# Kernel tuning notes

Hardware: AMD Instinct MI355X
Metric: run time of the kernel (lower is better)

## Reference

```python
import jax, jax.numpy as jnp
import numpy as np

B, S, H = 8, 2048, 768      # batch, seq_len, hidden_size
N = 512                     # spans per example
MAXW = 30                   # max span width (length in [0, MAXW-1] -> width <= MAXW)


def setup_inputs() -> dict:
    key = jax.random.key(0)
    k1, k2, k3, k4 = jax.random.split(key, 4)
    embeddings = jax.random.normal(k1, (B, S, H), dtype=jnp.float32)
    starts = jax.random.randint(k2, (B, N), 0, S - MAXW)          # span starts
    lengths = jax.random.randint(k3, (B, N), 0, MAXW)             # end = start + length
    w = jax.random.normal(k4, (H, 1), dtype=jnp.float32) * 0.02   # nn.Linear(hidden, 1) weight (transposed)
    b = jnp.zeros((1,), dtype=jnp.float32)                        # linear bias
    return {"embeddings": embeddings, "w": w, "b": b, "starts": starts, "lengths": lengths}


def reference(embeddings, w, b, starts, lengths):
    # Vectorized ragged span pooling: gather up to MAXW tokens per span,
    # masked softmax over attention scores, then concat [start, end, attn].
    ends = starts + lengths                                  # inclusive end index
    offs = jnp.arange(MAXW)                                  # (W,)
    positions = starts[..., None] + offs                     # (B, N, W)
    mask = offs[None, None, :] <= lengths[..., None]         # (B, N, W) valid-token mask

    gather = jax.vmap(lambda e, p: e[p])                     # per-example gather
    span_emb = gather(embeddings, positions)                 # (B, N, W, H)

    scores = span_emb @ w + b                                # (B, N, W, 1)
    scores = jnp.where(mask[..., None], scores, -jnp.inf)
    attn_w = jax.nn.softmax(scores, axis=2)                  # masked softmax over span width
    attn_out = jnp.sum(attn_w * span_emb, axis=2)            # (B, N, H)

    start_emb = gather(embeddings, starts)                   # (B, N, H)
    end_emb = gather(embeddings, ends)                       # (B, N, H)
    return jnp.concatenate([start_emb, end_emb, attn_out], axis=-1)  # (B, N, 3H)
```

## Files before the change

### kernel.cpp

```cpp
#include <hip/hip_runtime.h>
#include <hip/hip_bf16.h>
#include <math.h>

#define BB 8
#define SS 2048
#define HH 768
#define NN 512
#define MAXW 30
#define CK 6

__global__ __launch_bounds__(256) void sort_spans_kernel(
    const int* __restrict__ starts,
    int*       __restrict__ order)
{
    const int b   = blockIdx.x;
    const int tid = threadIdx.x;
    __shared__ int hist[SS];
    __shared__ int wsum[4];

    for (int i = tid; i < SS; i += 256) hist[i] = 0;
    __syncthreads();

    const int* st = starts + b * NN;
    for (int n = tid; n < NN; n += 256) atomicAdd(&hist[st[n]], 1);
    __syncthreads();

    const int base = tid * 8;
    int cnt[8]; int s = 0;
    #pragma unroll
    for (int k = 0; k < 8; ++k) { cnt[k] = hist[base + k]; s += cnt[k]; }

    const int lane = tid & 63, wv = tid >> 6;
    int v = s;
    #pragma unroll
    for (int off = 1; off < 64; off <<= 1) {
        int u = __shfl_up(v, off);
        if (lane >= off) v += u;
    }
    if (lane == 63) wsum[wv] = v;
    __syncthreads();
    int wbase = 0;
    #pragma unroll
    for (int k = 0; k < 4; ++k) wbase += (k < wv) ? wsum[k] : 0;

    int excl = wbase + v - s;
    #pragma unroll
    for (int k = 0; k < 8; ++k) { int c = cnt[k]; hist[base + k] = excl; excl += c; }
    __syncthreads();

    for (int n = tid; n < NN; n += 256) {
        int pos = atomicAdd(&hist[st[n]], 1);
        order[b * NN + pos] = n;
    }
}

__global__ __launch_bounds__(256) void span_fused_kernel(
    const float* __restrict__ emb,
    const float* __restrict__ w,
    const float* __restrict__ bias,
    const int*   __restrict__ starts,
    const int*   __restrict__ lengths,
    const int*   __restrict__ order,
    float*       __restrict__ out)
{
    const int tid  = threadIdx.x;
    const int wv   = tid >> 6;
    const int lane = tid & 63;
    const int bi   = blockIdx.x & 7;
    const int rank = ((int)blockIdx.x >> 3) * 4 + wv;
    const int n    = order ? order[bi * NN + rank] : rank;
    const int span = bi * NN + n;

    const int start = starts[span];
    const int len   = lengths[span];

    const float* ebase = emb + (size_t)bi * SS * HH + (size_t)start * HH;
    const int h0 = lane * 4;
    float* orow = out + (size_t)span * (3 * HH);

    const float4 w0 = *reinterpret_cast<const float4*>(w + h0);
    const float4 w1 = *reinterpret_cast<const float4*>(w + h0 + 256);
    const float4 w2 = *reinterpret_cast<const float4*>(w + h0 + 512);
    const float bb = bias[0];

    float m = -INFINITY, ssum = 0.f;
    float4 a0 = make_float4(0.f, 0.f, 0.f, 0.f), a1 = a0, a2 = a0;

    const int nchunks = (len + CK) / CK;

    for (int c = 0; c < nchunks; ++c) {
        const int tbase = c * CK;

        float4 r0[CK], r1[CK], r2[CK];
        #pragma unroll
        for (int k = 0; k < CK; ++k) {
            const float* rp = ebase + (size_t)(tbase + k) * HH;
            r0[k] = *reinterpret_cast<const float4*>(rp + h0);
            r1[k] = *reinterpret_cast<const float4*>(rp + h0 + 256);
            r2[k] = *reinterpret_cast<const float4*>(rp + h0 + 512);
        }

        float d[CK];
        #pragma unroll
        for (int k = 0; k < CK; ++k) {
            d[k] = r0[k].x * w0.x + r0[k].y * w0.y + r0[k].z * w0.z + r0[k].w * w0.w
                 + r1[k].x * w1.x + r1[k].y * w1.y + r1[k].z * w1.z + r1[k].w * w1.w
                 + r2[k].x * w2.x + r2[k].y * w2.y + r2[k].z * w2.z + r2[k].w * w2.w;
        }

        #pragma unroll
        for (int off = 32; off; off >>= 1) {
            #pragma unroll
            for (int k = 0; k < CK; ++k) d[k] += __shfl_xor(d[k], off);
        }

        #pragma unroll
        for (int k = 0; k < CK; ++k)
            d[k] = (tbase + k <= len) ? (d[k] + bb) : -INFINITY;

        float cmax = d[0];
        #pragma unroll
        for (int k = 1; k < CK; ++k) cmax = fmaxf(cmax, d[k]);
        if (cmax > m) {
            const float cc = __expf(m - cmax);
            ssum *= cc;
            a0.x *= cc; a0.y *= cc; a0.z *= cc; a0.w *= cc;
            a1.x *= cc; a1.y *= cc; a1.z *= cc; a1.w *= cc;
            a2.x *= cc; a2.y *= cc; a2.z *= cc; a2.w *= cc;
            m = cmax;
        }

        #pragma unroll
        for (int k = 0; k < CK; ++k) {
            const float pt = __expf(d[k] - m);
            ssum += pt;
            a0.x += pt * r0[k].x; a0.y += pt * r0[k].y; a0.z += pt * r0[k].z; a0.w += pt * r0[k].w;
            a1.x += pt * r1[k].x; a1.y += pt * r1[k].y; a1.z += pt * r1[k].z; a1.w += pt * r1[k].w;
            a2.x += pt * r2[k].x; a2.y += pt * r2[k].y; a2.z += pt * r2[k].z; a2.w += pt * r2[k].w;

            if (tbase + k == 0) {
                *reinterpret_cast<float4*>(orow + h0)       = r0[k];
                *reinterpret_cast<float4*>(orow + h0 + 256) = r1[k];
                *reinterpret_cast<float4*>(orow + h0 + 512) = r2[k];
            }
            if (tbase + k == len) {
                *reinterpret_cast<float4*>(orow + HH + h0)       = r0[k];
                *reinterpret_cast<float4*>(orow + HH + h0 + 256) = r1[k];
                *reinterpret_cast<float4*>(orow + HH + h0 + 512) = r2[k];
            }
        }
    }

    const float inv = 1.f / ssum;
    a0.x *= inv; a0.y *= inv; a0.z *= inv; a0.w *= inv;
    a1.x *= inv; a1.y *= inv; a1.z *= inv; a1.w *= inv;
    a2.x *= inv; a2.y *= inv; a2.z *= inv; a2.w *= inv;
    *reinterpret_cast<float4*>(orow + 2 * HH + h0)       = a0;
    *reinterpret_cast<float4*>(orow + 2 * HH + h0 + 256) = a1;
    *reinterpret_cast<float4*>(orow + 2 * HH + h0 + 512) = a2;
}

extern "C" void kernel_launch(void* const* d_in, const int* in_sizes, int n_in,
                              void* d_out, int out_size, void* d_ws, size_t ws_size,
                              hipStream_t stream) {
    const float* emb     = (const float*)d_in[0];
    const float* w       = (const float*)d_in[1];
    const float* bias    = (const float*)d_in[2];
    const int*   starts  = (const int*)d_in[3];
    const int*   lengths = (const int*)d_in[4];
    float*       out     = (float*)d_out;

    int* order = nullptr;
    if (ws_size >= (size_t)(BB * NN * sizeof(int))) {
        order = (int*)d_ws;
        sort_spans_kernel<<<dim3(BB), dim3(256), 0, stream>>>(starts, order);
    }

    span_fused_kernel<<<dim3(BB * NN / 4), dim3(256), 0, stream>>>(
        emb, w, bias, starts, lengths, order, out);
}
```

Measured before the change: 34.87 us.

## Group 8 sorted spans per block and sweep their shared token union in lockstep

Each block now handles 8 start-sorted spans (one per wave, 512 threads) instead of 4. The block computes the min start and max end over its spans, and all waves step over that token range together in chunks of 4, with a block barrier after each chunk. Each wave loads only tokens inside its own span, so overlapping spans hit the same rows close together in time, which should raise cache reuse. In exchange, waves whose spans are short or far apart run many empty iterations and wait at every barrier. The chunk shrinks from 6 to 4 tokens, which reduces memory-level parallelism per wave.

```diff
diff --git a/kernel.cpp b/kernel.cpp
--- a/kernel.cpp
+++ b/kernel.cpp
@@ -7,7 +7,8 @@
 #define HH 768
 #define NN 512
 #define MAXW 30
-#define CK 6
+#define SPW 8
+#define CH  4
 
 __global__ __launch_bounds__(256) void sort_spans_kernel(
     const int* __restrict__ starts,
@@ -54,7 +55,7 @@
     }
 }
 
-__global__ __launch_bounds__(256) void span_fused_kernel(
+__global__ __launch_bounds__(512, 4) void span_union_kernel(
     const float* __restrict__ emb,
     const float* __restrict__ w,
     const float* __restrict__ bias,
@@ -67,14 +68,23 @@
     const int wv   = tid >> 6;
     const int lane = tid & 63;
     const int bi   = blockIdx.x & 7;
-    const int rank = ((int)blockIdx.x >> 3) * 4 + wv;
+    const int g    = (int)blockIdx.x >> 3;
+    const int rank = g * SPW + wv;
     const int n    = order ? order[bi * NN + rank] : rank;
     const int span = bi * NN + n;
 
     const int start = starts[span];
     const int len   = lengths[span];
-
-    const float* ebase = emb + (size_t)bi * SS * HH + (size_t)start * HH;
+    const int end   = start + len;
+
+    __shared__ int s_lo[SPW], s_hi[SPW];
+    if (lane == 0) { s_lo[wv] = start; s_hi[wv] = end; }
+    __syncthreads();
+    int wlo = s_lo[0], whi = s_hi[0];
+    #pragma unroll
+    for (int k = 1; k < SPW; ++k) { wlo = min(wlo, s_lo[k]); whi = max(whi, s_hi[k]); }
+
+    const float* ebase = emb + (size_t)bi * SS * HH;
     const int h0 = lane * 4;
     float* orow = out + (size_t)span * (3 * HH);
 
@@ -86,41 +96,47 @@
     float m = -INFINITY, ssum = 0.f;
     float4 a0 = make_float4(0.f, 0.f, 0.f, 0.f), a1 = a0, a2 = a0;
 
-    const int nchunks = (len + CK) / CK;
-
-    for (int c = 0; c < nchunks; ++c) {
-        const int tbase = c * CK;
-
-        float4 r0[CK], r1[CK], r2[CK];
-        #pragma unroll
-        for (int k = 0; k < CK; ++k) {
-            const float* rp = ebase + (size_t)(tbase + k) * HH;
-            r0[k] = *reinterpret_cast<const float4*>(rp + h0);
-            r1[k] = *reinterpret_cast<const float4*>(rp + h0 + 256);
-            r2[k] = *reinterpret_cast<const float4*>(rp + h0 + 512);
-        }
-
-        float d[CK];
-        #pragma unroll
-        for (int k = 0; k < CK; ++k) {
-            d[k] = r0[k].x * w0.x + r0[k].y * w0.y + r0[k].z * w0.z + r0[k].w * w0.w
-                 + r1[k].x * w1.x + r1[k].y * w1.y + r1[k].z * w1.z + r1[k].w * w1.w
-                 + r2[k].x * w2.x + r2[k].y * w2.y + r2[k].z * w2.z + r2[k].w * w2.w;
+    const int nch = (whi - wlo) / CH + 1;
+
+    for (int c = 0; c < nch; ++c) {
+        const int clo = wlo + c * CH;
+
+        float4 r0[CH], r1[CH], r2[CH];
+        bool val[CH];
+        #pragma unroll
+        for (int k = 0; k < CH; ++k) {
+            const int t = clo + k;
+            val[k] = (t >= start) && (t <= end);
+            if (val[k]) {
+                const float* rp = ebase + (size_t)t * HH + h0;
+                r0[k] = *reinterpret_cast<const float4*>(rp);
+                r1[k] = *reinterpret_cast<const float4*>(rp + 256);
+                r2[k] = *reinterpret_cast<const float4*>(rp + 512);
+            }
+        }
+
+        float d[CH];
+        #pragma unroll
+        for (int k = 0; k < CH; ++k) {
+            d[k] = val[k]
+                 ? (r0[k].x * w0.x + r0[k].y * w0.y + r0[k].z * w0.z + r0[k].w * w0.w
+                  + r1[k].x * w1.x + r1[k].y * w1.y + r1[k].z * w1.z + r1[k].w * w1.w
+                  + r2[k].x * w2.x + r2[k].y * w2.y + r2[k].z * w2.z + r2[k].w * w2.w)
+                 : 0.f;
         }
 
         #pragma unroll
         for (int off = 32; off; off >>= 1) {
             #pragma unroll
-            for (int k = 0; k < CK; ++k) d[k] += __shfl_xor(d[k], off);
-        }
-
-        #pragma unroll
-        for (int k = 0; k < CK; ++k)
-            d[k] = (tbase + k <= len) ? (d[k] + bb) : -INFINITY;
+            for (int k = 0; k < CH; ++k) d[k] += __shfl_xor(d[k], off);
+        }
+        #pragma unroll
+        for (int k = 0; k < CH; ++k)
+            d[k] = val[k] ? (d[k] + bb) : -INFINITY;
 
         float cmax = d[0];
         #pragma unroll
-        for (int k = 1; k < CK; ++k) cmax = fmaxf(cmax, d[k]);
+        for (int k = 1; k < CH; ++k) cmax = fmaxf(cmax, d[k]);
         if (cmax > m) {
             const float cc = __expf(m - cmax);
             ssum *= cc;
@@ -131,24 +147,29 @@
         }
 
         #pragma unroll
-        for (int k = 0; k < CK; ++k) {
-            const float pt = __expf(d[k] - m);
-            ssum += pt;
-            a0.x += pt * r0[k].x; a0.y += pt * r0[k].y; a0.z += pt * r0[k].z; a0.w += pt * r0[k].w;
-            a1.x += pt * r1[k].x; a1.y += pt * r1[k].y; a1.z += pt * r1[k].z; a1.w += pt * r1[k].w;
-            a2.x += pt * r2[k].x; a2.y += pt * r2[k].y; a2.z += pt * r2[k].z; a2.w += pt * r2[k].w;
-
-            if (tbase + k == 0) {
-                *reinterpret_cast<float4*>(orow + h0)       = r0[k];
-                *reinterpret_cast<float4*>(orow + h0 + 256) = r1[k];
-                *reinterpret_cast<float4*>(orow + h0 + 512) = r2[k];
+        for (int k = 0; k < CH; ++k) {
+            if (val[k]) {
+                const float pt = __expf(d[k] - m);
+                ssum += pt;
+                a0.x += pt * r0[k].x; a0.y += pt * r0[k].y; a0.z += pt * r0[k].z; a0.w += pt * r0[k].w;
+                a1.x += pt * r1[k].x; a1.y += pt * r1[k].y; a1.z += pt * r1[k].z; a1.w += pt * r1[k].w;
+                a2.x += pt * r2[k].x; a2.y += pt * r2[k].y; a2.z += pt * r2[k].z; a2.w += pt * r2[k].w;
+
+                const int t = clo + k;
+                if (t == start) {
+                    *reinterpret_cast<float4*>(orow + h0)       = r0[k];
+                    *reinterpret_cast<float4*>(orow + h0 + 256) = r1[k];
+                    *reinterpret_cast<float4*>(orow + h0 + 512) = r2[k];
+                }
+                if (t == end) {
+                    *reinterpret_cast<float4*>(orow + HH + h0)       = r0[k];
+                    *reinterpret_cast<float4*>(orow + HH + h0 + 256) = r1[k];
+                    *reinterpret_cast<float4*>(orow + HH + h0 + 512) = r2[k];
+                }
             }
-            if (tbase + k == len) {
-                *reinterpret_cast<float4*>(orow + HH + h0)       = r0[k];
-                *reinterpret_cast<float4*>(orow + HH + h0 + 256) = r1[k];
-                *reinterpret_cast<float4*>(orow + HH + h0 + 512) = r2[k];
-            }
-        }
+        }
+
+        __syncthreads();
     }
 
     const float inv = 1.f / ssum;
@@ -176,6 +197,6 @@
         sort_spans_kernel<<<dim3(BB), dim3(256), 0, stream>>>(starts, order);
     }
 
-    span_fused_kernel<<<dim3(BB * NN / 4), dim3(256), 0, stream>>>(
+    span_union_kernel<<<dim3(BB * NN / SPW), dim3(512), 0, stream>>>(
         emb, w, bias, starts, lengths, order, out);
 }
```

Result: slower. 53.77 us (+54.2%).
